# Performance work log

Measured on AMD Instinct MI355X. Metric: run time of the kernel, lower is better.

Reference implementation:

```python
import jax, jax.numpy as jnp
import numpy as np

RADIUS = 0.5
K = 32  # num_neighbor


def ball_query(distances, radius, k):
    # distances: (B, M, N) squared distances; mark points outside radius with N,
    # then sort indices so in-range points (in original order) come first.
    B, M, N = distances.shape
    idx = jnp.where(distances >= radius ** 2, N,
                    jnp.arange(N, dtype=jnp.int32)[None, None, :])
    return jnp.sort(idx, axis=-1)[:, :, :k]  # (B, M, k), padded with N


def setup_inputs() -> dict:
    key = jax.random.key(0)
    ks = jax.random.split(key, 6)
    B, N, M, D, C = 4, 16384, 1024, 3, 64
    C_op, C_out = 64, 128
    positions = jax.random.normal(ks[0], (B, N, D), jnp.float32)
    features = jax.random.normal(ks[1], (B, N, C), jnp.float32)
    centers = jax.random.normal(ks[2], (B, M, D), jnp.float32)
    distances = jax.random.uniform(ks[3], (B, M, N), dtype=jnp.float32)
    W_op = jax.random.normal(ks[4], (D + C, C_op), jnp.float32) * 0.05
    b_op = jnp.zeros((C_op,), jnp.float32)
    W_agg = jax.random.normal(ks[5], (C_op, C_out), jnp.float32) * 0.05
    b_agg = jnp.zeros((C_out,), jnp.float32)
    return {"positions": positions, "features": features, "centers": centers,
            "distances": distances, "W_op": W_op, "b_op": b_op,
            "W_agg": W_agg, "b_agg": b_agg}


def reference(positions, features, centers, distances, W_op, b_op, W_agg, b_agg):
    B, N, D = positions.shape
    ids = ball_query(distances, RADIUS, K)      # (B, M, K); N marks invalid slot
    mask = ids != N                             # valid neighbor mask
    safe = jnp.where(mask, ids, 0)
    bidx = jnp.arange(B)[:, None, None]
    pos_n = positions[bidx, safe]               # (B, M, K, D) neighbor gather
    feat_n = features[bidx, safe]               # (B, M, K, C)
    rel = pos_n - centers[:, :, None, :]        # relative coordinates
    # NeighborOperator: pointwise linear on [rel_pos, features]
    f = jnp.concatenate([rel, feat_n], axis=-1) @ W_op + b_op  # (B, M, K, C_op)
    # invalid slots map to the zeros row in the torch index_put trick
    f = jnp.where(mask[..., None], f, 0.0)
    pooled = jnp.max(f, axis=2)                 # neighbor max-pool (B, M, C_op)
    # Conv1dBlock with kernel 1 == per-center linear + relu
    return jax.nn.relu(pooled @ W_agg + b_agg)  # (B, M, out_channels)
```

## Files before the change

kernel.cpp:

```cpp
#include <hip/hip_runtime.h>

constexpr int B_    = 4;
constexpr int N_    = 16384;
constexpr int M_    = 1024;
constexpr int C_    = 64;
constexpr int COP_  = 64;
constexpr int COUT_ = 128;
constexpr int K_    = 32;
constexpr float R2_ = 0.25f;

__global__ __launch_bounds__(64) void pointnet_fused(
    const float* __restrict__ positions,
    const float* __restrict__ features,
    const float* __restrict__ centers,
    const float* __restrict__ distances,
    const float* __restrict__ W_op,
    const float* __restrict__ b_op,
    const float* __restrict__ W_agg,
    const float* __restrict__ b_agg,
    float* __restrict__ out)
{
    const int lane = threadIdx.x;
    const int bm   = blockIdx.x;
    const int b    = bm >> 10;
    const int bN   = b * N_;

    __shared__ int s_ids[K_];
    if (lane < K_) s_ids[lane] = 0;

    const float* drow = distances + (size_t)bm * N_;
    int found = 0;
    for (int n0 = 0; n0 < N_ && found < K_; n0 += 64) {
        const float d = drow[n0 + lane];
        const bool pred = d < R2_;
        const unsigned long long m = __ballot(pred);
        const int rank = found + __popcll(m & ((1ull << lane) - 1ull));
        if (pred && rank < K_) s_ids[rank] = n0 + lane;
        found += (int)__popcll(m);
    }
    const int valid = found < K_ ? found : K_;

    float w[67];
    #pragma unroll
    for (int c = 0; c < 67; ++c) w[c] = W_op[c * COP_ + lane];
    const float bop  = b_op[lane];
    const float ctr0 = centers[bm * 3 + 0];
    const float ctr1 = centers[bm * 3 + 1];
    const float ctr2 = centers[bm * 3 + 2];

    const int myid = s_ids[lane & (K_ - 1)];

    float pooled = -INFINITY;
    #pragma unroll
    for (int k = 0; k < K_; ++k) {
        const int id = __builtin_amdgcn_readlane(myid, k);
        const float*  pp = positions + (size_t)(bN + id) * 3;
        const float4* f4 = (const float4*)(features + (size_t)(bN + id) * C_);
        float acc = bop;
        acc = fmaf(pp[0] - ctr0, w[0], acc);
        acc = fmaf(pp[1] - ctr1, w[1], acc);
        acc = fmaf(pp[2] - ctr2, w[2], acc);
        #pragma unroll
        for (int c4 = 0; c4 < 16; ++c4) {
            const float4 x = f4[c4];
            acc = fmaf(x.x, w[3 + 4 * c4 + 0], acc);
            acc = fmaf(x.y, w[3 + 4 * c4 + 1], acc);
            acc = fmaf(x.z, w[3 + 4 * c4 + 2], acc);
            acc = fmaf(x.w, w[3 + 4 * c4 + 3], acc);
        }
        pooled = (k < valid) ? fmaxf(pooled, acc) : pooled;
    }
    if (valid < K_) pooled = fmaxf(pooled, 0.0f);

    float a0 = b_agg[lane];
    float a1 = b_agg[lane + 64];
    #pragma unroll
    for (int jj = 0; jj < COP_; ++jj) {
        const float p = __int_as_float(
            __builtin_amdgcn_readlane(__float_as_int(pooled), jj));
        a0 = fmaf(p, W_agg[jj * COUT_ + lane],      a0);
        a1 = fmaf(p, W_agg[jj * COUT_ + lane + 64], a1);
    }
    float* orow = out + (size_t)bm * COUT_;
    orow[lane]      = fmaxf(a0, 0.0f);
    orow[lane + 64] = fmaxf(a1, 0.0f);
}

extern "C" void kernel_launch(void* const* d_in, const int* in_sizes, int n_in,
                              void* d_out, int out_size, void* d_ws, size_t ws_size,
                              hipStream_t stream) {
    const float* positions = (const float*)d_in[0];
    const float* features  = (const float*)d_in[1];
    const float* centers   = (const float*)d_in[2];
    const float* distances = (const float*)d_in[3];
    const float* W_op      = (const float*)d_in[4];
    const float* b_op      = (const float*)d_in[5];
    const float* W_agg     = (const float*)d_in[6];
    const float* b_agg     = (const float*)d_in[7];
    float* out = (float*)d_out;

    dim3 grid(B_ * M_);
    dim3 block(64);
    pointnet_fused<<<grid, block, 0, stream>>>(
        positions, features, centers, distances,
        W_op, b_op, W_agg, b_agg, out);
}
```

Before: 352.9 us.

## Use bf16 MFMA for neighbor linear and prefetch first distance chunks

Replaces the per-lane scalar FMA loop over 32 neighbors with two 32x32x16 bf16 MFMA tiles, where each lane gathers part of a neighbor feature row and converts it to bf16. The row-wise max-pool is then done from the accumulator layout with a cross-half shuffle. It also loads the first four distance chunks up front so the ball-query loop does not serialize on those loads. This targets FMA-bound compute and serialized per-neighbor gathers, but converting inputs and weights to bf16 loses precision, and W_op is reconverted per block.

```diff
diff --git a/kernel.cpp b/kernel.cpp
--- a/kernel.cpp
+++ b/kernel.cpp
@@ -8,6 +8,15 @@
 constexpr int COUT_ = 128;
 constexpr int K_    = 32;
 constexpr float R2_ = 0.25f;
+
+typedef __attribute__((ext_vector_type(8)))  short bf16x8;
+typedef __attribute__((ext_vector_type(16))) float f32x16;
+
+static __device__ __forceinline__ short f2bf(float f) {
+    union { float f; unsigned u; } v; v.f = f;
+    const unsigned r = v.u + 0x7fffu + ((v.u >> 16) & 1u);
+    return (short)(r >> 16);
+}
 
 __global__ __launch_bounds__(64) void pointnet_fused(
     const float* __restrict__ positions,
@@ -29,57 +38,110 @@
     if (lane < K_) s_ids[lane] = 0;
 
     const float* drow = distances + (size_t)bm * N_;
+    float dch[4];
+    #pragma unroll
+    for (int i = 0; i < 4; ++i) dch[i] = drow[64 * i + lane];
+    const unsigned long long ltmask = (1ull << lane) - 1ull;
     int found = 0;
-    for (int n0 = 0; n0 < N_ && found < K_; n0 += 64) {
+    #pragma unroll
+    for (int i = 0; i < 4; ++i) {
+        const bool pred = dch[i] < R2_;
+        const unsigned long long mi = __ballot(pred);
+        const int rank = found + __popcll(mi & ltmask);
+        if (pred && rank < K_) s_ids[rank] = 64 * i + lane;
+        found += (int)__popcll(mi);
+    }
+    for (int n0 = 256; n0 < N_ && found < K_; n0 += 64) {
         const float d = drow[n0 + lane];
         const bool pred = d < R2_;
-        const unsigned long long m = __ballot(pred);
-        const int rank = found + __popcll(m & ((1ull << lane) - 1ull));
+        const unsigned long long mi = __ballot(pred);
+        const int rank = found + __popcll(mi & ltmask);
         if (pred && rank < K_) s_ids[rank] = n0 + lane;
-        found += (int)__popcll(m);
+        found += (int)__popcll(mi);
     }
     const int valid = found < K_ ? found : K_;
 
-    float w[67];
-    #pragma unroll
-    for (int c = 0; c < 67; ++c) w[c] = W_op[c * COP_ + lane];
-    const float bop  = b_op[lane];
     const float ctr0 = centers[bm * 3 + 0];
     const float ctr1 = centers[bm * 3 + 1];
     const float ctr2 = centers[bm * 3 + 2];
 
-    const int myid = s_ids[lane & (K_ - 1)];
+    const int rowid = s_ids[lane & (K_ - 1)];
+    const int koff  = (lane >> 5) * 8;
 
-    float pooled = -INFINITY;
+    const float* frow = features + (size_t)(bN + rowid) * C_;
+    float4 xa[8];
     #pragma unroll
-    for (int k = 0; k < K_; ++k) {
-        const int id = __builtin_amdgcn_readlane(myid, k);
-        const float*  pp = positions + (size_t)(bN + id) * 3;
-        const float4* f4 = (const float4*)(features + (size_t)(bN + id) * C_);
-        float acc = bop;
-        acc = fmaf(pp[0] - ctr0, w[0], acc);
-        acc = fmaf(pp[1] - ctr1, w[1], acc);
-        acc = fmaf(pp[2] - ctr2, w[2], acc);
+    for (int s = 0; s < 4; ++s) {
+        xa[2 * s]     = *(const float4*)(frow + 16 * s + koff);
+        xa[2 * s + 1] = *(const float4*)(frow + 16 * s + koff + 4);
+    }
+    const float* prow = positions + (size_t)(bN + rowid) * 3;
+    const float r0 = prow[0] - ctr0;
+    const float r1 = prow[1] - ctr1;
+    const float r2 = prow[2] - ctr2;
+
+    bf16x8 afr[5];
+    #pragma unroll
+    for (int s = 0; s < 4; ++s) {
+        afr[s][0] = f2bf(xa[2 * s].x);     afr[s][1] = f2bf(xa[2 * s].y);
+        afr[s][2] = f2bf(xa[2 * s].z);     afr[s][3] = f2bf(xa[2 * s].w);
+        afr[s][4] = f2bf(xa[2 * s + 1].x); afr[s][5] = f2bf(xa[2 * s + 1].y);
+        afr[s][6] = f2bf(xa[2 * s + 1].z); afr[s][7] = f2bf(xa[2 * s + 1].w);
+    }
+    #pragma unroll
+    for (int j = 0; j < 8; ++j) afr[4][j] = 0;
+    if (koff == 0) { afr[4][0] = f2bf(r0); afr[4][1] = f2bf(r1); afr[4][2] = f2bf(r2); }
+
+    const int n0col = lane & 31;
+    bf16x8 bfr[2][5];
+    #pragma unroll
+    for (int t = 0; t < 2; ++t) {
+        const int n = 32 * t + n0col;
         #pragma unroll
-        for (int c4 = 0; c4 < 16; ++c4) {
-            const float4 x = f4[c4];
-            acc = fmaf(x.x, w[3 + 4 * c4 + 0], acc);
-            acc = fmaf(x.y, w[3 + 4 * c4 + 1], acc);
-            acc = fmaf(x.z, w[3 + 4 * c4 + 2], acc);
-            acc = fmaf(x.w, w[3 + 4 * c4 + 3], acc);
+        for (int s = 0; s < 4; ++s)
+            #pragma unroll
+            for (int j = 0; j < 8; ++j)
+                bfr[t][s][j] = f2bf(W_op[(3 + 16 * s + koff + j) * COP_ + n]);
+        #pragma unroll
+        for (int j = 0; j < 8; ++j) {
+            const int c = koff + j;
+            bfr[t][4][j] = (c < 3) ? f2bf(W_op[c * COP_ + n]) : (short)0;
         }
-        pooled = (k < valid) ? fmaxf(pooled, acc) : pooled;
     }
-    if (valid < K_) pooled = fmaxf(pooled, 0.0f);
+
+    f32x16 acc0, acc1;
+    #pragma unroll
+    for (int i = 0; i < 16; ++i) { acc0[i] = 0.0f; acc1[i] = 0.0f; }
+    #pragma unroll
+    for (int s = 0; s < 5; ++s) {
+        acc0 = __builtin_amdgcn_mfma_f32_32x32x16_bf16(afr[s], bfr[0][s], acc0, 0, 0, 0);
+        acc1 = __builtin_amdgcn_mfma_f32_32x32x16_bf16(afr[s], bfr[1][s], acc1, 0, 0, 0);
+    }
+
+    const float bb0 = b_op[n0col];
+    const float bb1 = b_op[32 + n0col];
+    const int mbase = 4 * (lane >> 5);
+    float p0 = -INFINITY, p1 = -INFINITY;
+    #pragma unroll
+    for (int r = 0; r < 16; ++r) {
+        const int m = (r & 3) + 8 * (r >> 2) + mbase;
+        const bool ok = m < valid;
+        p0 = fmaxf(p0, ok ? (acc0[r] + bb0) : 0.0f);
+        p1 = fmaxf(p1, ok ? (acc1[r] + bb1) : 0.0f);
+    }
+    p0 = fmaxf(p0, __shfl_xor(p0, 32));
+    p1 = fmaxf(p1, __shfl_xor(p1, 32));
 
     float a0 = b_agg[lane];
     float a1 = b_agg[lane + 64];
     #pragma unroll
-    for (int jj = 0; jj < COP_; ++jj) {
-        const float p = __int_as_float(
-            __builtin_amdgcn_readlane(__float_as_int(pooled), jj));
-        a0 = fmaf(p, W_agg[jj * COUT_ + lane],      a0);
-        a1 = fmaf(p, W_agg[jj * COUT_ + lane + 64], a1);
+    for (int jj = 0; jj < 32; ++jj) {
+        const float q0 = __int_as_float(__builtin_amdgcn_readlane(__float_as_int(p0), jj));
+        a0 = fmaf(q0, W_agg[jj * COUT_ + lane],      a0);
+        a1 = fmaf(q0, W_agg[jj * COUT_ + lane + 64], a1);
+        const float q1 = __int_as_float(__builtin_amdgcn_readlane(__float_as_int(p1), jj));
+        a0 = fmaf(q1, W_agg[(32 + jj) * COUT_ + lane],      a0);
+        a1 = fmaf(q1, W_agg[(32 + jj) * COUT_ + lane + 64], a1);
     }
     float* orow = out + (size_t)bm * COUT_;
     orow[lane]      = fmaxf(a0, 0.0f);
```

Result: faster. 326.6 us (-7.5%).
